# Performance work log

Measured on AMD Instinct MI355X. Metric: run time of the kernel, lower is better.

The kernel has to match this reference:

```python
import jax, jax.numpy as jnp
import numpy as np

IN_DIM = 128
OUT_DIM = 256
NUM_F = 8
BATCH = 1024
NUM = IN_DIM * OUT_DIM


def setup_inputs() -> dict:
    key = jax.random.key(0)
    k_x, k_coef, k_bias = jax.random.split(key, 3)
    x = jax.random.normal(k_x, (BATCH, IN_DIM), dtype=jnp.float32)
    grid = jnp.arange(NUM_F, dtype=jnp.float32) + 1.0                      # [num_f]
    coef = jax.random.uniform(k_coef, (NUM, NUM_F), dtype=jnp.float32)     # torch.rand
    scale_base = jnp.ones((NUM,), dtype=jnp.float32)
    scale_sp = jnp.ones((NUM,), dtype=jnp.float32)
    # nn.Linear(out_dim, 1, bias=False).weight has shape [1, out_dim]
    bound = 1.0 / np.sqrt(OUT_DIM)
    bias_w = jax.random.uniform(k_bias, (1, OUT_DIM), dtype=jnp.float32,
                                minval=-bound, maxval=bound)
    return {"x": x, "grid": grid, "coef": coef, "scale_sp": scale_sp,
            "scale_base": scale_base, "bias_w": bias_w}


def reference(x, grid, coef, scale_sp, scale_base, bias_w):
    batch, in_dim = x.shape
    out_dim = bias_w.shape[1]
    num = in_dim * out_dim
    # Replicate x across out_dim: xe[b, o*in_dim + i] = x[b, i]  -> [batch, num]
    xe = jnp.broadcast_to(x[:, None, :], (batch, out_dim, in_dim)).reshape(batch, num)
    base = jax.nn.silu(xe)                                   # [batch, num]
    # sin(grid * x) basis expansion: [batch, num, num_f]
    f = jnp.sin(xe[:, :, None] * grid[None, None, :])
    fout = jnp.einsum('nf,bnf->bn', coef, f)                 # [batch, num]
    fout = scale_sp * fout + scale_base * base               # [batch, num]
    y = fout.reshape(batch, out_dim, in_dim).sum(axis=2)     # [batch, out_dim]
    return y + bias_w                                        # broadcast [1, out_dim]
```

## Files before the change

kernel.cpp:

```cpp
#include <hip/hip_runtime.h>
#include <hip/hip_bf16.h>

#define BATCH   1024
#define IN_DIM  128
#define OUT_DIM 256
#define NUM_F   8

#define BM 32
#define BN 32
#define BK 32
#define NCHUNK 36

#define XPAD 129
#define APAD 40

typedef __attribute__((ext_vector_type(8))) short short8;
typedef __attribute__((ext_vector_type(4))) float float4v;

static __device__ __forceinline__ unsigned short f2bf(float f) {
    union { float f; unsigned u; } v; v.f = f;
    unsigned r = v.u + 0x7FFFu + ((v.u >> 16) & 1u);
    return (unsigned short)(r >> 16);
}

__global__ __launch_bounds__(256)
void slayer_kernel(const float* __restrict__ x,
                   const float* __restrict__ coef,
                   const float* __restrict__ scale_sp,
                   const float* __restrict__ scale_base,
                   const float* __restrict__ bias_w,
                   float* __restrict__ y)
{
    __shared__ float x_lds[BM * XPAD];
    __shared__ short A_lds[BM * APAD];
    __shared__ short B_lds[BN * APAD];

    const int t  = threadIdx.x;
    const int o0 = blockIdx.x * BN;
    const int b0 = blockIdx.y * BM;

    {
        const float4v* xg = (const float4v*)(x + b0 * IN_DIM);
        #pragma unroll
        for (int r = 0; r < 4; ++r) {
            int flat = r * 1024 + t * 4;
            int b = flat >> 7, i = flat & 127;
            float4v v = xg[r * 256 + t];
            x_lds[b * XPAD + i + 0] = v.x;
            x_lds[b * XPAD + i + 1] = v.y;
            x_lds[b * XPAD + i + 2] = v.z;
            x_lds[b * XPAD + i + 3] = v.w;
        }
    }
    __syncthreads();

    const int wave = t >> 6;
    const int lane = t & 63;
    const int mrow = lane & 15;
    const int q    = lane >> 4;
    const int mw   = (wave & 1) * 16;
    const int nw   = (wave >> 1) * 16;

    float4v acc = {0.f, 0.f, 0.f, 0.f};

    for (int c = 0; c < NCHUNK; ++c) {
        if (c < 32) {
            const int i0 = c * 4;
            if (t < 128) {
                int b = t >> 2, il = t & 3;
                float xv = x_lds[b * XPAD + i0 + il];
                float s1 = __sinf(xv), c1 = __cosf(xv);
                float c2 = 2.f * c1;
                float s2 = c2 * s1;
                float s3 = c2 * s2 - s1;
                float s4 = c2 * s3 - s2;
                float s5 = c2 * s4 - s3;
                float s6 = c2 * s5 - s4;
                float s7 = c2 * s6 - s5;
                float s8 = c2 * s7 - s6;
                short8 pk;
                pk[0] = f2bf(s1); pk[1] = f2bf(s2); pk[2] = f2bf(s3); pk[3] = f2bf(s4);
                pk[4] = f2bf(s5); pk[5] = f2bf(s6); pk[6] = f2bf(s7); pk[7] = f2bf(s8);
                *(short8*)&A_lds[b * APAD + il * 8] = pk;
            } else {
                int t2 = t - 128;
                int o = t2 >> 2, il = t2 & 3;
                int n = (o0 + o) * IN_DIM + i0 + il;
                float sp = scale_sp[n];
                const float4v* cg = (const float4v*)(coef + (size_t)n * NUM_F);
                float4v v0 = cg[0], v1 = cg[1];
                short8 pk;
                pk[0] = f2bf(v0.x * sp); pk[1] = f2bf(v0.y * sp);
                pk[2] = f2bf(v0.z * sp); pk[3] = f2bf(v0.w * sp);
                pk[4] = f2bf(v1.x * sp); pk[5] = f2bf(v1.y * sp);
                pk[6] = f2bf(v1.z * sp); pk[7] = f2bf(v1.w * sp);
                *(short8*)&B_lds[o * APAD + il * 8] = pk;
            }
        } else {
            const int i0 = (c - 32) * 32;
            if (t < 128) {
                int b = t >> 2, kk = (t & 3) * 8;
                short8 pk;
                #pragma unroll
                for (int j = 0; j < 8; ++j) {
                    float xv = x_lds[b * XPAD + i0 + kk + j];
                    float s  = xv / (1.f + __expf(-xv));
                    pk[j] = f2bf(s);
                }
                *(short8*)&A_lds[b * APAD + kk] = pk;
            } else {
                int t2 = t - 128;
                int o = t2 >> 2, kk = (t2 & 3) * 8;
                const float* sb = scale_base + (size_t)(o0 + o) * IN_DIM + i0 + kk;
                short8 pk;
                #pragma unroll
                for (int j = 0; j < 8; ++j) pk[j] = f2bf(sb[j]);
                *(short8*)&B_lds[o * APAD + kk] = pk;
            }
        }
        __syncthreads();

        short8 af = *(const short8*)&A_lds[(mw + mrow) * APAD + q * 8];
        short8 bf = *(const short8*)&B_lds[(nw + mrow) * APAD + q * 8];
        acc = __builtin_amdgcn_mfma_f32_16x16x32_bf16(af, bf, acc, 0, 0, 0);

        __syncthreads();
    }

    const int ocol = o0 + nw + mrow;
    const float bias = bias_w[ocol];
    #pragma unroll
    for (int r = 0; r < 4; ++r) {
        int brow = b0 + mw + q * 4 + r;
        y[(size_t)brow * OUT_DIM + ocol] = acc[r] + bias;
    }
}

extern "C" void kernel_launch(void* const* d_in, const int* in_sizes, int n_in,
                              void* d_out, int out_size, void* d_ws, size_t ws_size,
                              hipStream_t stream) {
    const float* x          = (const float*)d_in[0];
    const float* coef       = (const float*)d_in[2];
    const float* scale_sp   = (const float*)d_in[3];
    const float* scale_base = (const float*)d_in[4];
    const float* bias_w     = (const float*)d_in[5];
    float* y = (float*)d_out;

    dim3 grid(OUT_DIM / BN, BATCH / BM);
    slayer_kernel<<<grid, 256, 0, stream>>>(x, coef, scale_sp, scale_base, bias_w, y);
}
```

Before: 82.03 us.

## Build MFMA operands directly in registers, removing LDS staging and barriers

Each lane now computes its own sin-recurrence A fragment and loads its own coef/scale B fragment, then feeds them straight to the MFMA. This drops the A/B LDS staging buffers and both per-chunk __syncthreads. It also vectorizes the x tile store and uses a packed bf16x2 conversion. The cost is redundant work: each wave recomputes sin/silu for its rows and reloads coef for its columns, instead of splitting those jobs across the block's thread halves.

```diff
diff --git a/kernel.cpp b/kernel.cpp
--- a/kernel.cpp
+++ b/kernel.cpp
@@ -1,26 +1,23 @@
 #include <hip/hip_runtime.h>
 #include <hip/hip_bf16.h>
 
-#define BATCH   1024
 #define IN_DIM  128
 #define OUT_DIM 256
 #define NUM_F   8
+#define BATCH   1024
 
 #define BM 32
 #define BN 32
-#define BK 32
-#define NCHUNK 36
-
-#define XPAD 129
-#define APAD 40
+#define XPAD 132
 
 typedef __attribute__((ext_vector_type(8))) short short8;
 typedef __attribute__((ext_vector_type(4))) float float4v;
 
-static __device__ __forceinline__ unsigned short f2bf(float f) {
-    union { float f; unsigned u; } v; v.f = f;
-    unsigned r = v.u + 0x7FFFu + ((v.u >> 16) & 1u);
-    return (unsigned short)(r >> 16);
+static __device__ __forceinline__ unsigned pk2(float a, float b) {
+    float2 t; t.x = a; t.y = b;
+    __hip_bfloat162 h = __float22bfloat162_rn(t);
+    union { __hip_bfloat162 h; unsigned u; } v; v.h = h;
+    return v.u;
 }
 
 __global__ __launch_bounds__(256)
@@ -32,107 +29,88 @@
                    float* __restrict__ y)
 {
     __shared__ float x_lds[BM * XPAD];
-    __shared__ short A_lds[BM * APAD];
-    __shared__ short B_lds[BN * APAD];
 
     const int t  = threadIdx.x;
     const int o0 = blockIdx.x * BN;
     const int b0 = blockIdx.y * BM;
 
     {
-        const float4v* xg = (const float4v*)(x + b0 * IN_DIM);
+        const float4v* xg = (const float4v*)(x + (size_t)b0 * IN_DIM);
         #pragma unroll
         for (int r = 0; r < 4; ++r) {
-            int flat = r * 1024 + t * 4;
-            int b = flat >> 7, i = flat & 127;
-            float4v v = xg[r * 256 + t];
-            x_lds[b * XPAD + i + 0] = v.x;
-            x_lds[b * XPAD + i + 1] = v.y;
-            x_lds[b * XPAD + i + 2] = v.z;
-            x_lds[b * XPAD + i + 3] = v.w;
+            int idx = r * 256 + t;
+            int b = idx >> 5, i4 = idx & 31;
+            float4v v = xg[idx];
+            *(float4v*)&x_lds[b * XPAD + i4 * 4] = v;
         }
     }
     __syncthreads();
 
-    const int wave = t >> 6;
-    const int lane = t & 63;
-    const int mrow = lane & 15;
-    const int q    = lane >> 4;
-    const int mw   = (wave & 1) * 16;
-    const int nw   = (wave >> 1) * 16;
+    const int wave = t >> 6, lane = t & 63;
+    const int mrow = lane & 15, q = lane >> 4;
+    const int mw = (wave & 1) * 16, nw = (wave >> 1) * 16;
+    const int m  = mw + mrow;
+    const int nn = o0 + nw + mrow;
+
+    const float* xrow = &x_lds[m * XPAD];
 
     float4v acc = {0.f, 0.f, 0.f, 0.f};
 
-    for (int c = 0; c < NCHUNK; ++c) {
-        if (c < 32) {
-            const int i0 = c * 4;
-            if (t < 128) {
-                int b = t >> 2, il = t & 3;
-                float xv = x_lds[b * XPAD + i0 + il];
-                float s1 = __sinf(xv), c1 = __cosf(xv);
-                float c2 = 2.f * c1;
-                float s2 = c2 * s1;
-                float s3 = c2 * s2 - s1;
-                float s4 = c2 * s3 - s2;
-                float s5 = c2 * s4 - s3;
-                float s6 = c2 * s5 - s4;
-                float s7 = c2 * s6 - s5;
-                float s8 = c2 * s7 - s6;
-                short8 pk;
-                pk[0] = f2bf(s1); pk[1] = f2bf(s2); pk[2] = f2bf(s3); pk[3] = f2bf(s4);
-                pk[4] = f2bf(s5); pk[5] = f2bf(s6); pk[6] = f2bf(s7); pk[7] = f2bf(s8);
-                *(short8*)&A_lds[b * APAD + il * 8] = pk;
-            } else {
-                int t2 = t - 128;
-                int o = t2 >> 2, il = t2 & 3;
-                int n = (o0 + o) * IN_DIM + i0 + il;
-                float sp = scale_sp[n];
-                const float4v* cg = (const float4v*)(coef + (size_t)n * NUM_F);
-                float4v v0 = cg[0], v1 = cg[1];
-                short8 pk;
-                pk[0] = f2bf(v0.x * sp); pk[1] = f2bf(v0.y * sp);
-                pk[2] = f2bf(v0.z * sp); pk[3] = f2bf(v0.w * sp);
-                pk[4] = f2bf(v1.x * sp); pk[5] = f2bf(v1.y * sp);
-                pk[6] = f2bf(v1.z * sp); pk[7] = f2bf(v1.w * sp);
-                *(short8*)&B_lds[o * APAD + il * 8] = pk;
-            }
-        } else {
-            const int i0 = (c - 32) * 32;
-            if (t < 128) {
-                int b = t >> 2, kk = (t & 3) * 8;
-                short8 pk;
-                #pragma unroll
-                for (int j = 0; j < 8; ++j) {
-                    float xv = x_lds[b * XPAD + i0 + kk + j];
-                    float s  = xv / (1.f + __expf(-xv));
-                    pk[j] = f2bf(s);
-                }
-                *(short8*)&A_lds[b * APAD + kk] = pk;
-            } else {
-                int t2 = t - 128;
-                int o = t2 >> 2, kk = (t2 & 3) * 8;
-                const float* sb = scale_base + (size_t)(o0 + o) * IN_DIM + i0 + kk;
-                short8 pk;
-                #pragma unroll
-                for (int j = 0; j < 8; ++j) pk[j] = f2bf(sb[j]);
-                *(short8*)&B_lds[o * APAD + kk] = pk;
-            }
-        }
-        __syncthreads();
+    #pragma unroll 4
+    for (int c = 0; c < 32; ++c) {
+        const int i = c * 4 + q;
+        const size_t nidx = (size_t)nn * IN_DIM + i;
 
-        short8 af = *(const short8*)&A_lds[(mw + mrow) * APAD + q * 8];
-        short8 bf = *(const short8*)&B_lds[(nw + mrow) * APAD + q * 8];
-        acc = __builtin_amdgcn_mfma_f32_16x16x32_bf16(af, bf, acc, 0, 0, 0);
+        const float4v* cg = (const float4v*)(coef + nidx * NUM_F);
+        float4v c0 = cg[0], c1 = cg[1];
+        float sp = scale_sp[nidx];
 
-        __syncthreads();
+        float xv = xrow[i];
+        float s1 = __sinf(xv), cs = __cosf(xv);
+        float c2 = cs + cs;
+        float s2 = c2 * s1;
+        float s3 = c2 * s2 - s1;
+        float s4 = c2 * s3 - s2;
+        float s5 = c2 * s4 - s3;
+        float s6 = c2 * s5 - s4;
+        float s7 = c2 * s6 - s5;
+        float s8 = c2 * s7 - s6;
+
+        union { short8 s; unsigned u[4]; } af, bf;
+        af.u[0] = pk2(s1, s2); af.u[1] = pk2(s3, s4);
+        af.u[2] = pk2(s5, s6); af.u[3] = pk2(s7, s8);
+        bf.u[0] = pk2(c0.x * sp, c0.y * sp); bf.u[1] = pk2(c0.z * sp, c0.w * sp);
+        bf.u[2] = pk2(c1.x * sp, c1.y * sp); bf.u[3] = pk2(c1.z * sp, c1.w * sp);
+
+        acc = __builtin_amdgcn_mfma_f32_16x16x32_bf16(af.s, bf.s, acc, 0, 0, 0);
     }
 
-    const int ocol = o0 + nw + mrow;
-    const float bias = bias_w[ocol];
+    #pragma unroll
+    for (int c = 0; c < 4; ++c) {
+        const int i0 = c * 32 + q * 8;
+        float4v xa = *(const float4v*)&xrow[i0];
+        float4v xb = *(const float4v*)&xrow[i0 + 4];
+        const float4v* sb = (const float4v*)(scale_base + (size_t)nn * IN_DIM + i0);
+        float4v g0 = sb[0], g1 = sb[1];
+
+        float s[8] = {xa.x, xa.y, xa.z, xa.w, xb.x, xb.y, xb.z, xb.w};
+        #pragma unroll
+        for (int j = 0; j < 8; ++j) s[j] = s[j] / (1.f + __expf(-s[j]));
+
+        union { short8 s; unsigned u[4]; } af, bf;
+        af.u[0] = pk2(s[0], s[1]); af.u[1] = pk2(s[2], s[3]);
+        af.u[2] = pk2(s[4], s[5]); af.u[3] = pk2(s[6], s[7]);
+        bf.u[0] = pk2(g0.x, g0.y); bf.u[1] = pk2(g0.z, g0.w);
+        bf.u[2] = pk2(g1.x, g1.y); bf.u[3] = pk2(g1.z, g1.w);
+
+        acc = __builtin_amdgcn_mfma_f32_16x16x32_bf16(af.s, bf.s, acc, 0, 0, 0);
+    }
+
+    const float bias = bias_w[nn];
     #pragma unroll
     for (int r = 0; r < 4; ++r) {
         int brow = b0 + mw + q * 4 + r;
-        y[(size_t)brow * OUT_DIM + ocol] = acc[r] + bias;
+        y[(size_t)brow * OUT_DIM + nn] = acc[r] + bias;
     }
 }
 
```

After: 76.00 us. 7.3% less time.
